# Kernel tuning notes

Measured on AMD Instinct MI355X. Metric: run time of the kernel, lower is better.

The kernel has to match this reference:

```python
import jax, jax.numpy as jnp
import numpy as np

IN_DIM, HID, MEM, OUT = 512, 1024, 1024, 512
BATCH = 4096
HIST = 5  # hist_steps hard-coded in MMU.__init__

_LINEARS = [("inpgate", IN_DIM, HID), ("rec_inpgate", OUT, HID), ("mem_inpgate", MEM, HID),
            ("inp", IN_DIM, HID), ("rec_inp", OUT, HID),
            ("readgate", IN_DIM, MEM), ("rec_readgate", OUT, MEM), ("mem_readgate", MEM, MEM),
            ("decoder", HID, MEM),
            ("writegate", IN_DIM, MEM), ("rec_writegate", OUT, MEM), ("mem_writegate", MEM, MEM),
            ("encoder", MEM, HID)]


def setup_inputs() -> dict:
    key = jax.random.key(0)
    ks = iter(jax.random.split(key, 2 * len(_LINEARS) + 4))
    d = {"input": jax.random.normal(next(ks), (IN_DIM, BATCH), jnp.float32)}
    for name, fin, fout in _LINEARS:
        bound = 1.0 / np.sqrt(fin)  # torch nn.Linear default init range
        d["W_" + name] = jax.random.uniform(next(ks), (fout, fin), jnp.float32, -bound, bound)
        d["b_" + name] = jax.random.uniform(next(ks), (fout,), jnp.float32, -bound, bound)
    d["w_hid_out"] = jax.random.uniform(next(ks), (OUT, MEM), jnp.float32)  # torch.rand
    return d


def reference(input, W_inpgate, b_inpgate, W_rec_inpgate, b_rec_inpgate,
              W_mem_inpgate, b_mem_inpgate, W_inp, b_inp, W_rec_inp, b_rec_inp,
              W_readgate, b_readgate, W_rec_readgate, b_rec_readgate,
              W_mem_readgate, b_mem_readgate, W_decoder, b_decoder,
              W_writegate, b_writegate, W_rec_writegate, b_rec_writegate,
              W_mem_writegate, b_mem_writegate, W_encoder, b_encoder, w_hid_out):
    B = input.shape[1]
    lin = lambda x, W, b: x @ W.T + b
    # fresh module: history is zeros except last slot = current input (transposed to [B, in])
    xs = jnp.concatenate([jnp.zeros((HIST - 1, B, IN_DIM), input.dtype), input.T[None]], axis=0)

    def step(carry, x):
        out, mem = carry  # [B, OUT], [B, MEM]
        block_inp = jax.nn.sigmoid(lin(x, W_inp, b_inp) + lin(out, W_rec_inp, b_rec_inp))
        inp_gate = jax.nn.sigmoid(lin(x, W_inpgate, b_inpgate) + lin(mem, W_mem_inpgate, b_mem_inpgate)
                                  + lin(out, W_rec_inpgate, b_rec_inpgate))
        read_gate = jax.nn.sigmoid(lin(x, W_readgate, b_readgate) + lin(mem, W_mem_readgate, b_mem_readgate)
                                   + lin(out, W_rec_readgate, b_rec_readgate))
        decoded_mem = lin(read_gate * mem, W_decoder, b_decoder)
        hidden = decoded_mem + block_inp * inp_gate  # [B, HID] (HID == MEM)
        write_gate = jax.nn.sigmoid(lin(x, W_writegate, b_writegate) + lin(mem, W_mem_writegate, b_mem_writegate)
                                    + lin(out, W_rec_writegate, b_rec_writegate))
        encoded = jnp.tanh(lin(hidden, W_encoder, b_encoder))
        mem = (1.0 - write_gate) * mem + write_gate * encoded
        out = hidden @ w_hid_out.T  # w_hid_out.mm(hidden.T).T
        return (out, mem), None

    init = (jnp.zeros((B, OUT), input.dtype), jnp.zeros((B, MEM), input.dtype))
    (out, _mem), _ = jax.lax.scan(step, init, xs)
    return out
```

## Files before the change

### kernel.cpp

```cpp
#include <hip/hip_runtime.h>
#include <hip/hip_bf16.h>
#include <math.h>

typedef __hip_bfloat16 bf16;
typedef __attribute__((ext_vector_type(8))) short s16x8;
typedef __attribute__((ext_vector_type(4))) float f32x4;

__device__ __forceinline__ float fsig(float x) {
  return __builtin_amdgcn_rcpf(1.0f + __expf(-x));
}
__device__ __forceinline__ float ftanh(float x) { return 2.0f * fsig(2.0f * x) - 1.0f; }
__device__ __forceinline__ float dot4(float4 a, float4 b) {
  return a.x * b.x + a.y * b.y + a.z * b.z + a.w * b.w;
}
__device__ __forceinline__ float wred(float s) {
#pragma unroll
  for (int off = 32; off > 0; off >>= 1) s += __shfl_down(s, off, 64);
  return s;
}
__device__ __forceinline__ float b2f(unsigned short u) {
  return __uint_as_float((unsigned)u << 16);
}
__device__ __forceinline__ float4 b2f4(ushort4 u) {
  return make_float4(b2f(u.x), b2f(u.y), b2f(u.z), b2f(u.w));
}

__global__ void setup(const float* __restrict__ W_inp, const float* __restrict__ W_ig,
                      const float* __restrict__ W_rg, const float* __restrict__ W_ho,
                      const float* __restrict__ W_dec, const float* __restrict__ W_enc,
                      const float* __restrict__ input,
                      const float* __restrict__ b_inp, const float* __restrict__ b_rinp,
                      const float* __restrict__ b_ig, const float* __restrict__ b_mig,
                      const float* __restrict__ b_rig, const float* __restrict__ b_wg,
                      const float* __restrict__ b_mwg, const float* __restrict__ b_rwg,
                      const float* __restrict__ b_dec, const float* __restrict__ b_enc,
                      bf16* __restrict__ Wcat,
                      bf16* __restrict__ WhoB, bf16* __restrict__ Wcat2, bf16* __restrict__ Wdt,
                      bf16* __restrict__ WencB, bf16* __restrict__ Xb,
                      float* __restrict__ out_s, float* __restrict__ mem_s,
                      float* __restrict__ vout, float* __restrict__ Web) {
  __shared__ float t[32][33];
  const int id = blockIdx.x, tid = threadIdx.x;
  if (id < 12288) {
    const int i = id * 256 + tid;
    if (i < 524288) {
      Wcat[i] = __float2bfloat16(W_inp[i]);
    } else if (i < 1048576) {
      Wcat[i] = __float2bfloat16(W_ig[i - 524288]);
    } else if (i < 1572864) {
      Wcat[i] = __float2bfloat16(W_rg[i - 1048576]);
    } else if (i < 2097152) {
      const int k = i - 1572864;
      const bf16 vv = __float2bfloat16(W_ho[k]);
      WhoB[k] = vv;
      Wcat2[(size_t)(k >> 10) * 2048 + (k & 1023)] = vv;
    } else {
      const int k = i - 2097152;
      WencB[k] = __float2bfloat16(W_enc[k]);
    }
  } else if (id < 14336) {
    const int b = id - 12288;
    const int i0 = (b >> 7) * 32, b0 = (b & 127) * 32;
    const int tx = tid & 31, ty = tid >> 5;
#pragma unroll
    for (int r = ty; r < 32; r += 8) t[r][tx] = input[(size_t)(i0 + r) * 4096 + b0 + tx];
    __syncthreads();
#pragma unroll
    for (int r = ty; r < 32; r += 8)
      Xb[(size_t)(b0 + r) * 512 + i0 + tx] = __float2bfloat16(t[tx][r]);
  } else if (id < 15360) {
    const int b = id - 14336;
    const int j0 = (b >> 5) * 32, k0 = (b & 31) * 32;
    const int tx = tid & 31, ty = tid >> 5;
#pragma unroll
    for (int r = ty; r < 32; r += 8) t[r][tx] = W_dec[(size_t)(j0 + r) * 1024 + k0 + tx];
    __syncthreads();
#pragma unroll
    for (int r = ty; r < 32; r += 8)
      Wdt[(size_t)(k0 + r) * 1024 + j0 + tx] = __float2bfloat16(t[tx][r]);
  } else if (id < 16896) {
    const int o = id - 15360;
    const float* row = (o < 512) ? (W_ho + (size_t)o * 1024) : (W_enc + (size_t)(o - 512) * 1024);
    const float4 a = *(const float4*)(row + tid * 4);
    const float4 b = *(const float4*)(b_dec + tid * 4);
    float s = wred(dot4(a, b));
    if ((tid & 63) == 0) t[0][tid >> 6] = s;
    __syncthreads();
    if (tid == 0) {
      const float d = t[0][0] + t[0][1] + t[0][2] + t[0][3];
      if (o < 512) vout[o] = d;
      else Web[o - 512] = d;
    }
  } else {
    const int id2 = id - 16896;
    const float4 bd = *(const float4*)(b_dec + tid * 4);
    const float4 v1 = *(const float4*)(b_inp + tid * 4);
    const float4 v2 = *(const float4*)(b_rinp + tid * 4);
    const float4 v3 = *(const float4*)(b_ig + tid * 4);
    const float4 v4 = *(const float4*)(b_mig + tid * 4);
    const float4 v5 = *(const float4*)(b_rig + tid * 4);
    float4 hv;
    hv.x = bd.x + fsig(v1.x + v2.x) * fsig(v3.x + v4.x + v5.x);
    hv.y = bd.y + fsig(v1.y + v2.y) * fsig(v3.y + v4.y + v5.y);
    hv.z = bd.z + fsig(v1.z + v2.z) * fsig(v3.z + v4.z + v5.z);
    hv.w = bd.w + fsig(v1.w + v2.w) * fsig(v3.w + v4.w + v5.w);
    const float* row =
        (id2 < 1024) ? (W_enc + (size_t)id2 * 1024) : (W_ho + (size_t)(id2 - 1024) * 1024);
    float s = wred(dot4(*(const float4*)(row + tid * 4), hv));
    if ((tid & 63) == 0) t[0][tid >> 6] = s;
    __syncthreads();
    if (tid == 0) {
      const float d = t[0][0] + t[0][1] + t[0][2] + t[0][3];
      if (id2 < 1024) {
        const float wg = fsig(b_wg[id2] + b_mwg[id2] + b_rwg[id2]);
        mem_s[id2] = wg * ftanh(b_enc[id2] + d);
      } else {
        out_s[id2 - 1024] = d;
      }
    }
  }
}

__global__ __launch_bounds__(256) void gates_pe(
    const float* __restrict__ Wri, const float* __restrict__ Wmig,
    const float* __restrict__ Wrig, const float* __restrict__ Wmrg,
    const float* __restrict__ Wrrg, const float* __restrict__ Wmwg,
    const float* __restrict__ Wrwg, const float* __restrict__ b_inp,
    const float* __restrict__ b_rinp, const float* __restrict__ b_ig,
    const float* __restrict__ b_mig, const float* __restrict__ b_rig,
    const float* __restrict__ b_rg, const float* __restrict__ b_mrg,
    const float* __restrict__ b_rrg, const float* __restrict__ b_wg,
    const float* __restrict__ b_mwg, const float* __restrict__ b_rwg,
    const float* __restrict__ out_s, const float* __restrict__ mem_s,
    float* __restrict__ rgm, float* __restrict__ h0v, float* __restrict__ wgv,
    const bf16* __restrict__ WhoB, const bf16* __restrict__ WencB,
    const bf16* __restrict__ Wdt, bf16* __restrict__ Pb, bf16* __restrict__ Eb,
    int pe_blocks) {
  __shared__ char smem[32768];
  const int tid = threadIdx.x;
  if ((int)blockIdx.x >= pe_blocks) {
    float(*red)[4] = (float(*)[4])smem;
    const int j = blockIdx.x - pe_blocks, lane = tid & 63, wave = tid >> 6;
    const float4 z = make_float4(0.f, 0.f, 0.f, 0.f);
    const float4 o4 = (tid < 128) ? *(const float4*)(out_s + tid * 4) : z;
    const float4 m4 = *(const float4*)(mem_s + tid * 4);
    float p[7];
    p[0] = dot4((tid < 128) ? *(const float4*)(Wri + (size_t)j * 512 + tid * 4) : z, o4);
    p[1] = dot4(*(const float4*)(Wmig + (size_t)j * 1024 + tid * 4), m4);
    p[2] = dot4((tid < 128) ? *(const float4*)(Wrig + (size_t)j * 512 + tid * 4) : z, o4);
    p[3] = dot4(*(const float4*)(Wmrg + (size_t)j * 1024 + tid * 4), m4);
    p[4] = dot4((tid < 128) ? *(const float4*)(Wrrg + (size_t)j * 512 + tid * 4) : z, o4);
    p[5] = dot4(*(const float4*)(Wmwg + (size_t)j * 1024 + tid * 4), m4);
    p[6] = dot4((tid < 128) ? *(const float4*)(Wrwg + (size_t)j * 512 + tid * 4) : z, o4);
#pragma unroll
    for (int d = 0; d < 7; ++d) {
      float s = wred(p[d]);
      if (lane == 0) red[d][wave] = s;
    }
    __syncthreads();
    if (tid == 0) {
      float D[7];
#pragma unroll
      for (int d = 0; d < 7; ++d) D[d] = red[d][0] + red[d][1] + red[d][2] + red[d][3];
      const float abi = b_inp[j] + b_rinp[j] + D[0];
      const float aig = b_ig[j] + b_mig[j] + b_rig[j] + D[1] + D[2];
      const float arg = b_rg[j] + b_mrg[j] + b_rrg[j] + D[3] + D[4];
      const float awg = b_wg[j] + b_mwg[j] + b_rwg[j] + D[5] + D[6];
      rgm[j] = fsig(arg) * mem_s[j];
      h0v[j] = fsig(abi) * fsig(aig);
      wgv[j] = fsig(awg);
    }
    return;
  }
  const int bi = blockIdx.x;
  const bf16* Ag;
  bf16* Cg;
  int m0, n0;
  if (bi < 128) {
    Ag = WhoB; Cg = Pb;
    m0 = (bi >> 4) * 64; n0 = (bi & 15) * 64;
  } else {
    const int b2 = bi - 128;
    Ag = WencB; Cg = Eb;
    m0 = (b2 >> 4) * 64; n0 = (b2 & 15) * 64;
  }
  const int wave = tid >> 6, lane = tid & 63;
  const int wm = wave >> 1, wn = wave & 1;
  f32x4 acc[2][2] = {};

  auto STAGE = [&](int kt, unsigned bofs) {
#pragma unroll
    for (int i = 0; i < 2; ++i) {
      const int ci = i * 256 + tid;
      const int row = ci >> 3, ck = (ci & 7) ^ (row & 7);
      const bf16* g = Ag + (size_t)(m0 + row) * 1024 + kt + ck * 8;
      const unsigned lofs =
          (unsigned)__builtin_amdgcn_readfirstlane(bofs + (i * 256 + wave * 64) * 16);
      __builtin_amdgcn_global_load_lds(
          (const __attribute__((address_space(1))) void*)g,
          (__attribute__((address_space(3))) void*)(smem + lofs), 16, 0, 0);
    }
#pragma unroll
    for (int i = 0; i < 2; ++i) {
      const int ci = i * 256 + tid;
      const int row = ci >> 3, ck = (ci & 7) ^ (row & 7);
      const bf16* g = Wdt + (size_t)(n0 + row) * 1024 + kt + ck * 8;
      const unsigned lofs =
          (unsigned)__builtin_amdgcn_readfirstlane(bofs + 8192 + (i * 256 + wave * 64) * 16);
      __builtin_amdgcn_global_load_lds(
          (const __attribute__((address_space(1))) void*)g,
          (__attribute__((address_space(3))) void*)(smem + lofs), 16, 0, 0);
    }
  };

  STAGE(0, 0);
  __syncthreads();
  unsigned cur = 0;
  for (int kt = 0; kt < 1024; kt += 64) {
    if (kt + 64 < 1024) STAGE(kt + 64, (cur ^ 1u) * 16384u);
#pragma unroll
    for (int ks = 0; ks < 2; ++ks) {
      const int ckk = ks * 4 + (lane >> 4);
      const unsigned cofs = cur * 16384u;
      s16x8 af[2];
#pragma unroll
      for (int i = 0; i < 2; ++i) {
        const int R = wm * 32 + i * 16 + (lane & 15);
        af[i] = *(const s16x8*)(smem + cofs + (R * 8 + (ckk ^ (R & 7))) * 16);
      }
#pragma unroll
      for (int j = 0; j < 2; ++j) {
        const int R = wn * 32 + j * 16 + (lane & 15);
        const s16x8 bfr = *(const s16x8*)(smem + cofs + 8192 + (R * 8 + (ckk ^ (R & 7))) * 16);
#pragma unroll
        for (int i = 0; i < 2; ++i)
          acc[i][j] = __builtin_amdgcn_mfma_f32_16x16x32_bf16(af[i], bfr, acc[i][j], 0, 0, 0);
      }
    }
    __syncthreads();
    cur ^= 1u;
  }
  const int mb = (lane >> 4) * 4, nb = lane & 15;
#pragma unroll
  for (int i = 0; i < 2; ++i) {
#pragma unroll
    for (int j = 0; j < 2; ++j) {
      const int col = n0 + wn * 32 + j * 16 + nb;
#pragma unroll
      for (int r = 0; r < 4; ++r) {
        const int rowg = m0 + wm * 32 + i * 16 + mb + r;
        Cg[(size_t)rowg * 1024 + col] = __float2bfloat16(acc[i][j][r]);
      }
    }
  }
}

__global__ void step_fuse(const bf16* __restrict__ Eb, const bf16* __restrict__ WencB,
                          const bf16* __restrict__ Pb, const bf16* __restrict__ WhoB,
                          const float* __restrict__ b_enc, const float* __restrict__ Web,
                          const float* __restrict__ vout, const float* __restrict__ rgm,
                          const float* __restrict__ h0v, const float* __restrict__ wgv,
                          float* __restrict__ mem_s, float* __restrict__ out_s) {
  __shared__ float red[4];
  const int id = blockIdx.x, tid = threadIdx.x;
  const float4 r4 = *(const float4*)(rgm + tid * 4);
  const float4 h4 = *(const float4*)(h0v + tid * 4);
  const bf16* Ar = (id < 1024) ? (Eb + (size_t)id * 1024) : (Pb + (size_t)(id - 1024) * 1024);
  const bf16* Br =
      (id < 1024) ? (WencB + (size_t)id * 1024) : (WhoB + (size_t)(id - 1024) * 1024);
  const float4 a4 = b2f4(*(const ushort4*)(Ar + tid * 4));
  const float4 b4 = b2f4(*(const ushort4*)(Br + tid * 4));
  const float s = wred(dot4(a4, r4) + dot4(b4, h4));
  if ((tid & 63) == 0) red[tid >> 6] = s;
  __syncthreads();
  if (tid == 0) {
    const float d = red[0] + red[1] + red[2] + red[3];
    if (id < 1024) {
      const float wg = wgv[id];
      mem_s[id] = (1.0f - wg) * mem_s[id] + wg * ftanh(b_enc[id] + Web[id] + d);
    } else {
      out_s[id - 1024] = vout[id - 1024] + d;
    }
  }
}

__global__ void final_consts(const float* __restrict__ Wri, const float* __restrict__ Wmig,
                             const float* __restrict__ Wrig, const float* __restrict__ Wmrg,
                             const float* __restrict__ Wrrg, const float* __restrict__ b_inp,
                             const float* __restrict__ b_rinp, const float* __restrict__ b_ig,
                             const float* __restrict__ b_mig, const float* __restrict__ b_rig,
                             const float* __restrict__ b_rg, const float* __restrict__ b_mrg,
                             const float* __restrict__ b_rrg, const float* __restrict__ out_s,
                             const float* __restrict__ mem_s, const bf16* __restrict__ Pb,
                             float* __restrict__ ccat, bf16* __restrict__ Wcat2) {
  __shared__ float red[5][4];
  const int id = blockIdx.x, tid = threadIdx.x, lane = tid & 63, wave = tid >> 6;
  if (id < 1024) {
    const float4 z = make_float4(0.f, 0.f, 0.f, 0.f);
    const float4 o4 = (tid < 128) ? *(const float4*)(out_s + tid * 4) : z;
    const float4 m4 = *(const float4*)(mem_s + tid * 4);
    float p[5];
    p[0] = dot4((tid < 128) ? *(const float4*)(Wri + (size_t)id * 512 + tid * 4) : z, o4);
    p[1] = dot4(*(const float4*)(Wmig + (size_t)id * 1024 + tid * 4), m4);
    p[2] = dot4((tid < 128) ? *(const float4*)(Wrig + (size_t)id * 512 + tid * 4) : z, o4);
    p[3] = dot4(*(const float4*)(Wmrg + (size_t)id * 1024 + tid * 4), m4);
    p[4] = dot4((tid < 128) ? *(const float4*)(Wrrg + (size_t)id * 512 + tid * 4) : z, o4);
#pragma unroll
    for (int d = 0; d < 5; ++d) {
      float s = wred(p[d]);
      if (lane == 0) red[d][wave] = s;
    }
    __syncthreads();
    if (tid == 0) {
      float D[5];
#pragma unroll
      for (int d = 0; d < 5; ++d) D[d] = red[d][0] + red[d][1] + red[d][2] + red[d][3];
      ccat[id] = b_inp[id] + b_rinp[id] + D[0];
      ccat[1024 + id] = b_ig[id] + b_mig[id] + b_rig[id] + D[1] + D[2];
      ccat[2048 + id] = b_rg[id] + b_mrg[id] + b_rrg[id] + D[3] + D[4];
    }
  } else {
    const int idx = (id - 1024) * 256 + tid;
    const int k = idx & 1023;
    const float pv = b2f(((const unsigned short*)Pb)[idx]);
    Wcat2[(size_t)(idx >> 10) * 2048 + 1024 + k] = __float2bfloat16(pv * mem_s[k]);
  }
}

__global__ __launch_bounds__(256, 4) void gemm_gates(const bf16* __restrict__ A,
                                                     const bf16* __restrict__ Wcat,
                                                     const float* __restrict__ ccat,
                                                     bf16* __restrict__ Hcat) {
  __shared__ char smem[32768];
  const int tid = threadIdx.x, wave = tid >> 6, lane = tid & 63;
  const int wm = wave >> 1, wn = wave & 1;
  const int m0 = blockIdx.y * 64, n0 = blockIdx.x * 64;
  f32x4 acc[3][2][2] = {};

  for (int kt = 0; kt < 512; kt += 64) {
    __syncthreads();
#pragma unroll
    for (int i = 0; i < 2; ++i) {
      const int ci = i * 256 + tid;
      const int row = ci >> 3, ck = (ci & 7) ^ (row & 7);
      const bf16* g = A + (size_t)(m0 + row) * 512 + kt + ck * 8;
      const unsigned lofs = (unsigned)__builtin_amdgcn_readfirstlane((i * 256 + wave * 64) * 16);
      __builtin_amdgcn_global_load_lds(
          (const __attribute__((address_space(1))) void*)g,
          (__attribute__((address_space(3))) void*)(smem + lofs), 16, 0, 0);
    }
#pragma unroll
    for (int gI = 0; gI < 3; ++gI) {
      const bf16* Bp = Wcat + gI * 524288;
#pragma unroll
      for (int i = 0; i < 2; ++i) {
        const int ci = i * 256 + tid;
        const int row = ci >> 3, ck = (ci & 7) ^ (row & 7);
        const bf16* g = Bp + (size_t)(n0 + row) * 512 + kt + ck * 8;
        const unsigned lofs = (unsigned)__builtin_amdgcn_readfirstlane(
            8192 + gI * 8192 + (i * 256 + wave * 64) * 16);
        __builtin_amdgcn_global_load_lds(
            (const __attribute__((address_space(1))) void*)g,
            (__attribute__((address_space(3))) void*)(smem + lofs), 16, 0, 0);
      }
    }
    __syncthreads();

#pragma unroll
    for (int ks = 0; ks < 2; ++ks) {
      const int ckk = ks * 4 + (lane >> 4);
      s16x8 af[2];
#pragma unroll
      for (int i = 0; i < 2; ++i) {
        const int R = wm * 32 + i * 16 + (lane & 15);
        af[i] = *(const s16x8*)(smem + (R * 8 + (ckk ^ (R & 7))) * 16);
      }
#pragma unroll
      for (int gI = 0; gI < 3; ++gI) {
#pragma unroll
        for (int j = 0; j < 2; ++j) {
          const int R = wn * 32 + j * 16 + (lane & 15);
          const s16x8 bfr =
              *(const s16x8*)(smem + 8192 + gI * 8192 + (R * 8 + (ckk ^ (R & 7))) * 16);
#pragma unroll
          for (int i = 0; i < 2; ++i)
            acc[gI][i][j] =
                __builtin_amdgcn_mfma_f32_16x16x32_bf16(af[i], bfr, acc[gI][i][j], 0, 0, 0);
        }
      }
    }
  }

  __syncthreads();
  bf16* sm = (bf16*)smem;
  bf16* sr = (bf16*)smem + 5120;
  const int mb = (lane >> 4) * 4, nb = lane & 15;
#pragma unroll
  for (int i = 0; i < 2; ++i) {
#pragma unroll
    for (int j = 0; j < 2; ++j) {
      const int colL = wn * 32 + j * 16 + nb;
      const int jg = n0 + colL;
      const float c0 = ccat[jg], c1 = ccat[1024 + jg], c2 = ccat[2048 + jg];
#pragma unroll
      for (int r = 0; r < 4; ++r) {
        const int rowL = wm * 32 + i * 16 + mb + r;
        const float h = fsig(acc[0][i][j][r] + c0) * fsig(acc[1][i][j][r] + c1);
        const float rg = fsig(acc[2][i][j][r] + c2);
        sm[rowL * 80 + colL] = __float2bfloat16(h);
        sr[rowL * 80 + colL] = __float2bfloat16(rg);
      }
    }
  }
  __syncthreads();
#pragma unroll
  for (int pp = 0; pp < 2; ++pp) {
    const int c = pp * 256 + tid;
    const int row = c >> 3, cc = c & 7;
    const s16x8 v0 = *(const s16x8*)(sm + row * 80 + cc * 8);
    const s16x8 v1 = *(const s16x8*)(sr + row * 80 + cc * 8);
    *(s16x8*)(Hcat + (size_t)(m0 + row) * 2048 + n0 + cc * 8) = v0;
    *(s16x8*)(Hcat + (size_t)(m0 + row) * 2048 + 1024 + n0 + cc * 8) = v1;
  }
}

__global__ __launch_bounds__(256, 4) void gemm_out(const bf16* __restrict__ A,
                                                   const bf16* __restrict__ Bp,
                                                   const float* __restrict__ vout,
                                                   float* __restrict__ outF) {
  __shared__ char smem[32768];
  const int tid = threadIdx.x, wave = tid >> 6, lane = tid & 63;
  const int wm = wave >> 1, wn = wave & 1;
  const int m0 = blockIdx.y * 64, n0 = blockIdx.x * 64;
  f32x4 acc[2][2] = {};

  auto STAGE = [&](int kt, unsigned bofs) {
#pragma unroll
    for (int i = 0; i < 2; ++i) {
      const int ci = i * 256 + tid;
      const int row = ci >> 3, ck = (ci & 7) ^ (row & 7);
      const bf16* g = A + (size_t)(m0 + row) * 2048 + kt + ck * 8;
      const unsigned lofs =
          (unsigned)__builtin_amdgcn_readfirstlane(bofs + (i * 256 + wave * 64) * 16);
      __builtin_amdgcn_global_load_lds(
          (const __attribute__((address_space(1))) void*)g,
          (__attribute__((address_space(3))) void*)(smem + lofs), 16, 0, 0);
    }
#pragma unroll
    for (int i = 0; i < 2; ++i) {
      const int ci = i * 256 + tid;
      const int row = ci >> 3, ck = (ci & 7) ^ (row & 7);
      const bf16* g = Bp + (size_t)(n0 + row) * 2048 + kt + ck * 8;
      const unsigned lofs =
          (unsigned)__builtin_amdgcn_readfirstlane(bofs + 8192 + (i * 256 + wave * 64) * 16);
      __builtin_amdgcn_global_load_lds(
          (const __attribute__((address_space(1))) void*)g,
          (__attribute__((address_space(3))) void*)(smem + lofs), 16, 0, 0);
    }
  };

  STAGE(0, 0);
  __syncthreads();
  unsigned cur = 0;
  for (int kt = 0; kt < 2048; kt += 64) {
    if (kt + 64 < 2048) STAGE(kt + 64, (cur ^ 1u) * 16384u);
#pragma unroll
    for (int ks = 0; ks < 2; ++ks) {
      const int ckk = ks * 4 + (lane >> 4);
      const unsigned cofs = cur * 16384u;
      s16x8 af[2];
#pragma unroll
      for (int i = 0; i < 2; ++i) {
        const int R = wm * 32 + i * 16 + (lane & 15);
        af[i] = *(const s16x8*)(smem + cofs + (R * 8 + (ckk ^ (R & 7))) * 16);
      }
#pragma unroll
      for (int j = 0; j < 2; ++j) {
        const int R = wn * 32 + j * 16 + (lane & 15);
        const s16x8 bfr = *(const s16x8*)(smem + cofs + 8192 + (R * 8 + (ckk ^ (R & 7))) * 16);
#pragma unroll
        for (int i = 0; i < 2; ++i)
          acc[i][j] = __builtin_amdgcn_mfma_f32_16x16x32_bf16(af[i], bfr, acc[i][j], 0, 0, 0);
      }
    }
    __syncthreads();
    cur ^= 1u;
  }

  const int mb = (lane >> 4) * 4, nb = lane & 15;
#pragma unroll
  for (int i = 0; i < 2; ++i) {
#pragma unroll
    for (int j = 0; j < 2; ++j) {
      const int col = n0 + wn * 32 + j * 16 + nb;
#pragma unroll
      for (int r = 0; r < 4; ++r) {
        const int rowg = m0 + wm * 32 + i * 16 + mb + r;
        outF[(size_t)rowg * 512 + col] = acc[i][j][r] + vout[col];
      }
    }
  }
}

extern "C" void kernel_launch(void* const* d_in, const int* in_sizes, int n_in, void* d_out,
                              int out_size, void* d_ws, size_t ws_size, hipStream_t stream) {
  const float* input  = (const float*)d_in[0];
  const float* W_ig   = (const float*)d_in[1];  const float* b_ig   = (const float*)d_in[2];
  const float* W_rig  = (const float*)d_in[3];  const float* b_rig  = (const float*)d_in[4];
  const float* W_mig  = (const float*)d_in[5];  const float* b_mig  = (const float*)d_in[6];
  const float* W_inp  = (const float*)d_in[7];  const float* b_inp  = (const float*)d_in[8];
  const float* W_rinp = (const float*)d_in[9];  const float* b_rinp = (const float*)d_in[10];
  const float* W_rg   = (const float*)d_in[11]; const float* b_rg   = (const float*)d_in[12];
  const float* W_rrg  = (const float*)d_in[13]; const float* b_rrg  = (const float*)d_in[14];
  const float* W_mrg  = (const float*)d_in[15]; const float* b_mrg  = (const float*)d_in[16];
  const float* W_dec  = (const float*)d_in[17]; const float* b_dec  = (const float*)d_in[18];
  const float* W_wg   = (const float*)d_in[19]; const float* b_wg   = (const float*)d_in[20];
  const float* W_rwg  = (const float*)d_in[21]; const float* b_rwg  = (const float*)d_in[22];
  const float* W_mwg  = (const float*)d_in[23]; const float* b_mwg  = (const float*)d_in[24];
  const float* W_enc  = (const float*)d_in[25]; const float* b_enc  = (const float*)d_in[26];
  const float* W_ho   = (const float*)d_in[27];
  (void)W_wg;

  char* ws = (char*)d_ws;
  float* out_s = (float*)(ws + 0);
  float* mem_s = (float*)(ws + 4096);
  float* rgm   = (float*)(ws + 8192);
  float* h0v   = (float*)(ws + 12288);
  float* wgv   = (float*)(ws + 16384);
  float* ccat  = (float*)(ws + 24576);
  float* vout  = (float*)(ws + 40960);
  float* Web   = (float*)(ws + 45056);
  bf16* Pb     = (bf16*)(ws + 65536);
  bf16* Xb     = (bf16*)(ws + 2162688);
  bf16* Wcat   = (bf16*)(ws + 6356992);
  bf16* WhoB   = (bf16*)(ws + 9502720);
  bf16* Wcat2  = (bf16*)(ws + 10551296);
  bf16* Wdt    = (bf16*)(ws + 12648448);
  bf16* Hcat   = (bf16*)(ws + 14745600);
  bf16* Eb     = (bf16*)(ws + 31522816);
  bf16* WencB  = (bf16*)(ws + 35717120);

  setup<<<18432, 256, 0, stream>>>(W_inp, W_ig, W_rg, W_ho, W_dec, W_enc, input, b_inp, b_rinp,
                                   b_ig, b_mig, b_rig, b_wg, b_mwg, b_rwg, b_dec, b_enc, Wcat,
                                   WhoB, Wcat2, Wdt, WencB, Xb, out_s, mem_s, vout, Web);

  for (int s = 0; s < 3; ++s) {
    const int pe = (s == 0) ? 384 : 0;
    gates_pe<<<1024 + pe, 256, 0, stream>>>(W_rinp, W_mig, W_rig, W_mrg, W_rrg, W_mwg, W_rwg,
                                            b_inp, b_rinp, b_ig, b_mig, b_rig, b_rg, b_mrg,
                                            b_rrg, b_wg, b_mwg, b_rwg, out_s, mem_s, rgm, h0v,
                                            wgv, WhoB, WencB, Wdt, Pb, Eb, pe);
    step_fuse<<<1536, 256, 0, stream>>>(Eb, WencB, Pb, WhoB, b_enc, Web, vout, rgm, h0v, wgv,
                                        mem_s, out_s);
  }

  final_consts<<<3072, 256, 0, stream>>>(W_rinp, W_mig, W_rig, W_mrg, W_rrg, b_inp, b_rinp, b_ig,
                                         b_mig, b_rig, b_rg, b_mrg, b_rrg, out_s, mem_s, Pb,
                                         ccat, Wcat2);

  gemm_gates<<<dim3(16, 64), 256, 0, stream>>>(Xb, Wcat, ccat, Hcat);

  gemm_out<<<dim3(8, 64), 256, 0, stream>>>(Hcat, Wcat2, vout, (float*)d_out);
}
```

Before: 215.4 us.

## Pack recurrent gate weights to bf16 and double-buffer gemm_gates LDS tiles

Setup gets 5120 extra blocks that convert the seven recurrent/memory gate weight matrices into one interleaved bf16 buffer with row stride 5120. gates_pe runs three times and final_consts once; both now read this buffer instead of the fp32 originals, which halves their weight traffic. gemm_gates also moves to a two-stage LDS ping-pong, prefetching the next K tile while the current one feeds the MFMAs. The cost is a one-time conversion pass in setup and twice the shared memory in gemm_gates, whose launch bound drops from 4 blocks per CU, which may lower occupancy.

```diff
diff --git a/kernel.cpp b/kernel.cpp
--- a/kernel.cpp
+++ b/kernel.cpp
@@ -24,11 +24,17 @@
 __device__ __forceinline__ float4 b2f4(ushort4 u) {
   return make_float4(b2f(u.x), b2f(u.y), b2f(u.z), b2f(u.w));
 }
+
+#define WG7_STRIDE 5120
 
 __global__ void setup(const float* __restrict__ W_inp, const float* __restrict__ W_ig,
                       const float* __restrict__ W_rg, const float* __restrict__ W_ho,
                       const float* __restrict__ W_dec, const float* __restrict__ W_enc,
                       const float* __restrict__ input,
+                      const float* __restrict__ Wri, const float* __restrict__ Wmig,
+                      const float* __restrict__ Wrig, const float* __restrict__ Wmrg,
+                      const float* __restrict__ Wrrg, const float* __restrict__ Wmwg,
+                      const float* __restrict__ Wrwg,
                       const float* __restrict__ b_inp, const float* __restrict__ b_rinp,
                       const float* __restrict__ b_ig, const float* __restrict__ b_mig,
                       const float* __restrict__ b_rig, const float* __restrict__ b_wg,
@@ -38,7 +44,8 @@
                       bf16* __restrict__ WhoB, bf16* __restrict__ Wcat2, bf16* __restrict__ Wdt,
                       bf16* __restrict__ WencB, bf16* __restrict__ Xb,
                       float* __restrict__ out_s, float* __restrict__ mem_s,
-                      float* __restrict__ vout, float* __restrict__ Web) {
+                      float* __restrict__ vout, float* __restrict__ Web,
+                      bf16* __restrict__ Wg7) {
   __shared__ float t[32][33];
   const int id = blockIdx.x, tid = threadIdx.x;
   if (id < 12288) {
@@ -91,7 +98,7 @@
       if (o < 512) vout[o] = d;
       else Web[o - 512] = d;
     }
-  } else {
+  } else if (id < 18432) {
     const int id2 = id - 16896;
     const float4 bd = *(const float4*)(b_dec + tid * 4);
     const float4 v1 = *(const float4*)(b_inp + tid * 4);
@@ -118,14 +125,31 @@
         out_s[id2 - 1024] = d;
       }
     }
+  } else {
+    const int b = id - 18432;
+    const int j = b / 5, f = b - j * 5;
+    const int col = f * 1024 + tid * 4;
+    const float* src;
+    int c0, stride;
+    if (col < 512)       { src = Wri;  c0 = col;        stride = 512; }
+    else if (col < 1536) { src = Wmig; c0 = col - 512;  stride = 1024; }
+    else if (col < 2048) { src = Wrig; c0 = col - 1536; stride = 512; }
+    else if (col < 3072) { src = Wmrg; c0 = col - 2048; stride = 1024; }
+    else if (col < 3584) { src = Wrrg; c0 = col - 3072; stride = 512; }
+    else if (col < 4608) { src = Wmwg; c0 = col - 3584; stride = 1024; }
+    else                 { src = Wrwg; c0 = col - 4608; stride = 512; }
+    const float4 v = *(const float4*)(src + (size_t)j * stride + c0);
+    ushort4 u;
+    u.x = __bfloat16_as_ushort(__float2bfloat16(v.x));
+    u.y = __bfloat16_as_ushort(__float2bfloat16(v.y));
+    u.z = __bfloat16_as_ushort(__float2bfloat16(v.z));
+    u.w = __bfloat16_as_ushort(__float2bfloat16(v.w));
+    *(ushort4*)(Wg7 + (size_t)j * WG7_STRIDE + col) = u;
   }
 }
 
 __global__ __launch_bounds__(256) void gates_pe(
-    const float* __restrict__ Wri, const float* __restrict__ Wmig,
-    const float* __restrict__ Wrig, const float* __restrict__ Wmrg,
-    const float* __restrict__ Wrrg, const float* __restrict__ Wmwg,
-    const float* __restrict__ Wrwg, const float* __restrict__ b_inp,
+    const bf16* __restrict__ Wg7, const float* __restrict__ b_inp,
     const float* __restrict__ b_rinp, const float* __restrict__ b_ig,
     const float* __restrict__ b_mig, const float* __restrict__ b_rig,
     const float* __restrict__ b_rg, const float* __restrict__ b_mrg,
@@ -144,14 +168,15 @@
     const float4 z = make_float4(0.f, 0.f, 0.f, 0.f);
     const float4 o4 = (tid < 128) ? *(const float4*)(out_s + tid * 4) : z;
     const float4 m4 = *(const float4*)(mem_s + tid * 4);
+    const bf16* rowb = Wg7 + (size_t)j * WG7_STRIDE;
     float p[7];
-    p[0] = dot4((tid < 128) ? *(const float4*)(Wri + (size_t)j * 512 + tid * 4) : z, o4);
-    p[1] = dot4(*(const float4*)(Wmig + (size_t)j * 1024 + tid * 4), m4);
-    p[2] = dot4((tid < 128) ? *(const float4*)(Wrig + (size_t)j * 512 + tid * 4) : z, o4);
-    p[3] = dot4(*(const float4*)(Wmrg + (size_t)j * 1024 + tid * 4), m4);
-    p[4] = dot4((tid < 128) ? *(const float4*)(Wrrg + (size_t)j * 512 + tid * 4) : z, o4);
-    p[5] = dot4(*(const float4*)(Wmwg + (size_t)j * 1024 + tid * 4), m4);
-    p[6] = dot4((tid < 128) ? *(const float4*)(Wrwg + (size_t)j * 512 + tid * 4) : z, o4);
+    p[0] = (tid < 128) ? dot4(b2f4(*(const ushort4*)(rowb + tid * 4)), o4) : 0.f;
+    p[1] = dot4(b2f4(*(const ushort4*)(rowb + 512 + tid * 4)), m4);
+    p[2] = (tid < 128) ? dot4(b2f4(*(const ushort4*)(rowb + 1536 + tid * 4)), o4) : 0.f;
+    p[3] = dot4(b2f4(*(const ushort4*)(rowb + 2048 + tid * 4)), m4);
+    p[4] = (tid < 128) ? dot4(b2f4(*(const ushort4*)(rowb + 3072 + tid * 4)), o4) : 0.f;
+    p[5] = dot4(b2f4(*(const ushort4*)(rowb + 3584 + tid * 4)), m4);
+    p[6] = (tid < 128) ? dot4(b2f4(*(const ushort4*)(rowb + 4608 + tid * 4)), o4) : 0.f;
 #pragma unroll
     for (int d = 0; d < 7; ++d) {
       float s = wred(p[d]);
@@ -284,9 +309,7 @@
   }
 }
 
-__global__ void final_consts(const float* __restrict__ Wri, const float* __restrict__ Wmig,
-                             const float* __restrict__ Wrig, const float* __restrict__ Wmrg,
-                             const float* __restrict__ Wrrg, const float* __restrict__ b_inp,
+__global__ void final_consts(const bf16* __restrict__ Wg7, const float* __restrict__ b_inp,
                              const float* __restrict__ b_rinp, const float* __restrict__ b_ig,
                              const float* __restrict__ b_mig, const float* __restrict__ b_rig,
                              const float* __restrict__ b_rg, const float* __restrict__ b_mrg,
@@ -299,12 +322,13 @@
     const float4 z = make_float4(0.f, 0.f, 0.f, 0.f);
     const float4 o4 = (tid < 128) ? *(const float4*)(out_s + tid * 4) : z;
     const float4 m4 = *(const float4*)(mem_s + tid * 4);
+    const bf16* rowb = Wg7 + (size_t)id * WG7_STRIDE;
     float p[5];
-    p[0] = dot4((tid < 128) ? *(const float4*)(Wri + (size_t)id * 512 + tid * 4) : z, o4);
-    p[1] = dot4(*(const float4*)(Wmig + (size_t)id * 1024 + tid * 4), m4);
-    p[2] = dot4((tid < 128) ? *(const float4*)(Wrig + (size_t)id * 512 + tid * 4) : z, o4);
-    p[3] = dot4(*(const float4*)(Wmrg + (size_t)id * 1024 + tid * 4), m4);
-    p[4] = dot4((tid < 128) ? *(const float4*)(Wrrg + (size_t)id * 512 + tid * 4) : z, o4);
+    p[0] = (tid < 128) ? dot4(b2f4(*(const ushort4*)(rowb + tid * 4)), o4) : 0.f;
+    p[1] = dot4(b2f4(*(const ushort4*)(rowb + 512 + tid * 4)), m4);
+    p[2] = (tid < 128) ? dot4(b2f4(*(const ushort4*)(rowb + 1536 + tid * 4)), o4) : 0.f;
+    p[3] = dot4(b2f4(*(const ushort4*)(rowb + 2048 + tid * 4)), m4);
+    p[4] = (tid < 128) ? dot4(b2f4(*(const ushort4*)(rowb + 3072 + tid * 4)), o4) : 0.f;
 #pragma unroll
     for (int d = 0; d < 5; ++d) {
       float s = wred(p[d]);
@@ -327,24 +351,24 @@
   }
 }
 
-__global__ __launch_bounds__(256, 4) void gemm_gates(const bf16* __restrict__ A,
-                                                     const bf16* __restrict__ Wcat,
-                                                     const float* __restrict__ ccat,
-                                                     bf16* __restrict__ Hcat) {
-  __shared__ char smem[32768];
+__global__ __launch_bounds__(256) void gemm_gates(const bf16* __restrict__ A,
+                                                  const bf16* __restrict__ Wcat,
+                                                  const float* __restrict__ ccat,
+                                                  bf16* __restrict__ Hcat) {
+  __shared__ char smem[65536];
   const int tid = threadIdx.x, wave = tid >> 6, lane = tid & 63;
   const int wm = wave >> 1, wn = wave & 1;
   const int m0 = blockIdx.y * 64, n0 = blockIdx.x * 64;
   f32x4 acc[3][2][2] = {};
 
-  for (int kt = 0; kt < 512; kt += 64) {
-    __syncthreads();
+  auto STAGE = [&](int kt, unsigned bofs) {
 #pragma unroll
     for (int i = 0; i < 2; ++i) {
       const int ci = i * 256 + tid;
       const int row = ci >> 3, ck = (ci & 7) ^ (row & 7);
       const bf16* g = A + (size_t)(m0 + row) * 512 + kt + ck * 8;
-      const unsigned lofs = (unsigned)__builtin_amdgcn_readfirstlane((i * 256 + wave * 64) * 16);
+      const unsigned lofs =
+          (unsigned)__builtin_amdgcn_readfirstlane(bofs + (i * 256 + wave * 64) * 16);
       __builtin_amdgcn_global_load_lds(
           (const __attribute__((address_space(1))) void*)g,
           (__attribute__((address_space(3))) void*)(smem + lofs), 16, 0, 0);
@@ -358,22 +382,28 @@
         const int row = ci >> 3, ck = (ci & 7) ^ (row & 7);
         const bf16* g = Bp + (size_t)(n0 + row) * 512 + kt + ck * 8;
         const unsigned lofs = (unsigned)__builtin_amdgcn_readfirstlane(
-            8192 + gI * 8192 + (i * 256 + wave * 64) * 16);
+            bofs + 8192 + gI * 8192 + (i * 256 + wave * 64) * 16);
         __builtin_amdgcn_global_load_lds(
             (const __attribute__((address_space(1))) void*)g,
             (__attribute__((address_space(3))) void*)(smem + lofs), 16, 0, 0);
       }
     }
-    __syncthreads();
-
+  };
+
+  STAGE(0, 0);
+  __syncthreads();
+  unsigned cur = 0;
+  for (int kt = 0; kt < 512; kt += 64) {
+    if (kt + 64 < 512) STAGE(kt + 64, (cur ^ 1u) * 32768u);
 #pragma unroll
     for (int ks = 0; ks < 2; ++ks) {
       const int ckk = ks * 4 + (lane >> 4);
+      const unsigned cofs = cur * 32768u;
       s16x8 af[2];
 #pragma unroll
       for (int i = 0; i < 2; ++i) {
         const int R = wm * 32 + i * 16 + (lane & 15);
-        af[i] = *(const s16x8*)(smem + (R * 8 + (ckk ^ (R & 7))) * 16);
+        af[i] = *(const s16x8*)(smem + cofs + (R * 8 + (ckk ^ (R & 7))) * 16);
       }
 #pragma unroll
       for (int gI = 0; gI < 3; ++gI) {
@@ -381,7 +411,7 @@
         for (int j = 0; j < 2; ++j) {
           const int R = wn * 32 + j * 16 + (lane & 15);
           const s16x8 bfr =
-              *(const s16x8*)(smem + 8192 + gI * 8192 + (R * 8 + (ckk ^ (R & 7))) * 16);
+              *(const s16x8*)(smem + cofs + 8192 + gI * 8192 + (R * 8 + (ckk ^ (R & 7))) * 16);
 #pragma unroll
           for (int i = 0; i < 2; ++i)
             acc[gI][i][j] =
@@ -389,9 +419,10 @@
         }
       }
     }
-  }
-
-  __syncthreads();
+    __syncthreads();
+    cur ^= 1u;
+  }
+
   bf16* sm = (bf16*)smem;
   bf16* sr = (bf16*)smem + 5120;
   const int mb = (lane >> 4) * 4, nb = lane & 15;
@@ -539,24 +570,25 @@
   bf16* Hcat   = (bf16*)(ws + 14745600);
   bf16* Eb     = (bf16*)(ws + 31522816);
   bf16* WencB  = (bf16*)(ws + 35717120);
-
-  setup<<<18432, 256, 0, stream>>>(W_inp, W_ig, W_rg, W_ho, W_dec, W_enc, input, b_inp, b_rinp,
-                                   b_ig, b_mig, b_rig, b_wg, b_mwg, b_rwg, b_dec, b_enc, Wcat,
-                                   WhoB, Wcat2, Wdt, WencB, Xb, out_s, mem_s, vout, Web);
+  bf16* Wg7    = (bf16*)(ws + 37814272);
+
+  setup<<<23552, 256, 0, stream>>>(W_inp, W_ig, W_rg, W_ho, W_dec, W_enc, input,
+                                   W_rinp, W_mig, W_rig, W_mrg, W_rrg, W_mwg, W_rwg,
+                                   b_inp, b_rinp, b_ig, b_mig, b_rig, b_wg, b_mwg, b_rwg,
+                                   b_dec, b_enc, Wcat, WhoB, Wcat2, Wdt, WencB, Xb,
+                                   out_s, mem_s, vout, Web, Wg7);
 
   for (int s = 0; s < 3; ++s) {
     const int pe = (s == 0) ? 384 : 0;
-    gates_pe<<<1024 + pe, 256, 0, stream>>>(W_rinp, W_mig, W_rig, W_mrg, W_rrg, W_mwg, W_rwg,
-                                            b_inp, b_rinp, b_ig, b_mig, b_rig, b_rg, b_mrg,
+    gates_pe<<<1024 + pe, 256, 0, stream>>>(Wg7, b_inp, b_rinp, b_ig, b_mig, b_rig, b_rg, b_mrg,
                                             b_rrg, b_wg, b_mwg, b_rwg, out_s, mem_s, rgm, h0v,
                                             wgv, WhoB, WencB, Wdt, Pb, Eb, pe);
     step_fuse<<<1536, 256, 0, stream>>>(Eb, WencB, Pb, WhoB, b_enc, Web, vout, rgm, h0v, wgv,
                                         mem_s, out_s);
   }
 
-  final_consts<<<3072, 256, 0, stream>>>(W_rinp, W_mig, W_rig, W_mrg, W_rrg, b_inp, b_rinp, b_ig,
-                                         b_mig, b_rig, b_rg, b_mrg, b_rrg, out_s, mem_s, Pb,
-                                         ccat, Wcat2);
+  final_consts<<<3072, 256, 0, stream>>>(Wg7, b_inp, b_rinp, b_ig, b_mig, b_rig, b_rg, b_mrg,
+                                         b_rrg, out_s, mem_s, Pb, ccat, Wcat2);
 
   gemm_gates<<<dim3(16, 64), 256, 0, stream>>>(Xb, Wcat, ccat, Hcat);
 
```

After: 220.5 us. 2.4% more time.
